# Kernel tuning notes

Hardware: AMD Instinct MI355X
Metric: run time of the kernel (lower is better)

The kernel has to match this reference:

```python
import jax, jax.numpy as jnp
import numpy as np

B, N, F = 32, 1024, 7
HID, HID_GLO, MLP_H, OUT = 256, 8, 64, 8
THRESHOLD = 0.3


def setup_inputs() -> dict:
    key = jax.random.key(0)
    ks = jax.random.split(key, 16)
    def lin(k, fan_out, fan_in):
        # xavier-uniform-like init
        lim = (6.0 / (fan_in + fan_out)) ** 0.5
        return jax.random.uniform(k, (fan_out, fan_in), jnp.float32, -lim, lim)
    return {
        "x": jax.random.normal(ks[0], (B, N, F), jnp.float32),
        "W1": lin(ks[1], HID, 2),   "b1": jnp.zeros((HID,), jnp.float32),
        "W2": lin(ks[2], HID, HID), "b2": jnp.zeros((HID,), jnp.float32),
        "Wfc": lin(ks[3], HID, HID), "bfc": jnp.zeros((HID,), jnp.float32),
        "Wg": lin(ks[4], HID_GLO, 2), "bg": jnp.zeros((HID_GLO,), jnp.float32),
        "Wm0": lin(ks[5], MLP_H, N * F), "bm0": jnp.zeros((MLP_H,), jnp.float32),
        "Wm1": lin(ks[6], MLP_H, MLP_H), "bm1": jnp.zeros((MLP_H,), jnp.float32),
        "Wp": lin(ks[7], OUT, MLP_H + HID + HID_GLO), "bp": jnp.zeros((OUT,), jnp.float32),
    }


def reference(x, W1, b1, W2, b2, Wfc, bfc, Wg, bg, Wm0, bm0, Wm1, bm1, Wp, bp):
    # --- GCN branch (torch code detaches node features & adjacency) ---
    pts = jax.lax.stop_gradient(x[:, :, 1:3])                     # [B,N,2]
    diff = pts[:, :, None, :] - pts[:, None, :, :]                # [B,N,N,2]
    dist = jnp.sqrt(jnp.sum(diff * diff, axis=-1))                # [B,N,N]
    adj = (dist < THRESHOLD).astype(x.dtype)                      # [B,N,N]
    dinv = 1.0 / jnp.sqrt(jnp.sum(adj, axis=-1))                  # [B,N] (>=1, self-loop)
    nadj = dinv[:, :, None] * adj * dinv[:, None, :]              # D^-1/2 A D^-1/2
    h = jax.nn.relu(jnp.einsum('bij,bjd->bid', nadj, pts) @ W1.T + b1)   # [B,N,256]
    g = jnp.einsum('bij,bjh->bih', nadj, h) @ W2.T + b2                  # [B,N,256]
    gcn_en = jnp.mean(g, axis=1) @ Wfc.T + bfc                    # [B,256]

    # --- global branch (torch code uses .item() -> constants) ---
    v = jax.lax.stop_gradient(x[:, :, 1:5])                       # [B,N,4]
    avg_speed = jnp.mean(jnp.linalg.norm(v[:, :, 2:4], axis=-1), axis=1)  # [B]
    density = 1.0 / jnp.max(dist, axis=(1, 2))                    # [B] (v3 == pts)
    glo_in = jnp.stack([avg_speed, density], axis=-1)             # [B,2]
    glo_en = jax.nn.relu(glo_in @ Wg.T + bg)                      # [B,8]

    # --- MLP branch on flattened x ---
    xf = x.reshape(x.shape[0], -1)                                # [B, N*F]
    xf = jax.nn.relu(xf @ Wm0.T + bm0)
    xf = jax.nn.relu(xf @ Wm1.T + bm1)                            # [B,64]

    out = jnp.concatenate([xf, gcn_en, glo_en], axis=1) @ Wp.T + bp  # [B,8]
    return out
```

## Files before the change

### kernel.cpp

```cpp
#include <hip/hip_runtime.h>

#define NN 1024
#define FF 7
#define HID 256
#define MLPH 64
#define OUTN 8
#define CATN (MLPH + HID + 8)

__device__ __forceinline__ float wave_sum(float v) {
#pragma unroll
    for (int m = 32; m >= 1; m >>= 1) v += __shfl_xor(v, m, 64);
    return v;
}
__device__ __forceinline__ float wave_max(float v) {
#pragma unroll
    for (int m = 32; m >= 1; m >>= 1) v = fmaxf(v, __shfl_xor(v, m, 64));
    return v;
}

__global__ __launch_bounds__(512, 4) void g1(const float* __restrict__ x,
                                             const float* __restrict__ Wm0,
                                             const float* __restrict__ W2,
                                             const float* __restrict__ b2,
                                             const float* __restrict__ Wfc,
                                             const float* __restrict__ bfc,
                                             const float* __restrict__ Wp,
                                             float* __restrict__ spd,
                                             float* __restrict__ mlp_p,
                                             float* __restrict__ E,
                                             float* __restrict__ cE,
                                             float* __restrict__ deg,
                                             float* __restrict__ bmaxp,
                                             float* __restrict__ out) {
    __shared__ __align__(16) float l0[NN];
    __shared__ __align__(16) float l1[NN];
    __shared__ __align__(16) float s2[8 * 128];
    __shared__ float wred[8];
    __shared__ float eg0[HID];
    __shared__ float eg1[HID];
    int blk = blockIdx.x, tid = threadIdx.x, lane = tid & 63, w = tid >> 6;
    int b = blk >> 3, jg = blk & 7;
    const float* xb = x + b * (NN * FF);
    {
        int j0 = tid, j1 = tid + 512;
        l0[j0] = xb[j0 * FF + 1]; l1[j0] = xb[j0 * FF + 2];
        l0[j1] = xb[j1 * FF + 1]; l1[j1] = xb[j1 * FF + 2];
    }
    __syncthreads();
    int jA = jg * 128 + lane, jB = jA + 64;
    float pj0a = l0[jA], pj1a = l1[jA];
    float pj0b = l0[jB], pj1b = l1[jB];
    const float4* v0p = (const float4*)&l0[w * 128];
    const float4* v1p = (const float4*)&l1[w * 128];
    unsigned dA = 0u, dB = 0u;
    float mx = 0.f;
#pragma unroll 4
    for (int g = 0; g < 32; ++g) {
        float4 v0 = v0p[g], v1 = v1p[g];
        float dx, dy, d2a, d2b;
        dx = pj0a - v0.x; dy = pj1a - v1.x; d2a = fmaf(dy, dy, dx * dx);
        dx = pj0b - v0.x; dy = pj1b - v1.x; d2b = fmaf(dy, dy, dx * dx);
        dA += (d2a <= 0.09f); dB += (d2b <= 0.09f);
        mx = fmaxf(mx, fmaxf(d2a, d2b));
        dx = pj0a - v0.y; dy = pj1a - v1.y; d2a = fmaf(dy, dy, dx * dx);
        dx = pj0b - v0.y; dy = pj1b - v1.y; d2b = fmaf(dy, dy, dx * dx);
        dA += (d2a <= 0.09f); dB += (d2b <= 0.09f);
        mx = fmaxf(mx, fmaxf(d2a, d2b));
        dx = pj0a - v0.z; dy = pj1a - v1.z; d2a = fmaf(dy, dy, dx * dx);
        dx = pj0b - v0.z; dy = pj1b - v1.z; d2b = fmaf(dy, dy, dx * dx);
        dA += (d2a <= 0.09f); dB += (d2b <= 0.09f);
        mx = fmaxf(mx, fmaxf(d2a, d2b));
        dx = pj0a - v0.w; dy = pj1a - v1.w; d2a = fmaf(dy, dy, dx * dx);
        dx = pj0b - v0.w; dy = pj1b - v1.w; d2b = fmaf(dy, dy, dx * dx);
        dA += (d2a <= 0.09f); dB += (d2b <= 0.09f);
        mx = fmaxf(mx, fmaxf(d2a, d2b));
    }
    s2[w * 128 + lane] = (float)dA;
    s2[w * 128 + 64 + lane] = (float)dB;
    mx = wave_max(mx);
    if (lane == 0) wred[w] = mx;
    __syncthreads();
    if (tid < 128) {
        float s = 0.f;
#pragma unroll
        for (int kk = 0; kk < 8; ++kk) s += s2[kk * 128 + tid];
        deg[b * NN + jg * 128 + tid] = s;
    }
    if (tid == 0) {
        float m = wred[0];
#pragma unroll
        for (int i = 1; i < 8; ++i) m = fmaxf(m, wred[i]);
        bmaxp[b * 8 + jg] = m;
    }
    {
        int h = jg * 8 + w;
        const float4* wr = (const float4*)(Wm0 + h * (NN * FF));
        const float4* xr = (const float4*)xb;
        float4 a4 = {0.f, 0.f, 0.f, 0.f};
#pragma unroll 7
        for (int it = 0; it < 28; ++it) {
            float4 wv = wr[it * 64 + lane];
            float4 xv = xr[it * 64 + lane];
            a4.x = fmaf(wv.x, xv.x, a4.x);
            a4.y = fmaf(wv.y, xv.y, a4.y);
            a4.z = fmaf(wv.z, xv.z, a4.z);
            a4.w = fmaf(wv.w, xv.w, a4.w);
        }
        float s = (a4.x + a4.y) + (a4.z + a4.w);
        s = wave_sum(s);
        if (lane == 0) mlp_p[b * MLPH + h] = s;
    }
    __syncthreads();
    if (jg == 0) {
        int j0 = tid, j1 = tid + 512;
        float vx = xb[j0 * FF + 3], vy = xb[j0 * FF + 4];
        float sp = sqrtf(fmaf(vx, vx, vy * vy));
        vx = xb[j1 * FF + 3]; vy = xb[j1 * FF + 4];
        sp += sqrtf(fmaf(vx, vx, vy * vy));
        sp = wave_sum(sp);
        if (lane == 0) wred[w] = sp;
        if (tid < OUTN) out[b * OUTN + tid] = 0.f;
    }
    __syncthreads();
    if (jg == 0 && tid == 0) {
        float s = 0.f;
#pragma unroll
        for (int i = 0; i < 8; ++i) s += wred[i];
        spd[b] = s;
    }
    if (b < 8 && jg == 7) {
        int o = b;
        if (tid < HID) eg0[tid] = Wp[o * CATN + MLPH + tid];
        __syncthreads();
        if (tid < HID) {
            float a = 0.f;
#pragma unroll 8
            for (int m = 0; m < HID; ++m) a = fmaf(eg0[m], Wfc[m * HID + tid], a);
            eg1[tid] = a;
        }
        __syncthreads();
        if (tid < HID) {
            float e = 0.f;
#pragma unroll 8
            for (int k = 0; k < HID; ++k) e = fmaf(eg1[k], W2[k * HID + tid], e);
            E[o * HID + tid] = e;
            float c = fmaf(eg1[tid], b2[tid], eg0[tid] * bfc[tid]);
            c = wave_sum(c);
            if (lane == 0) wred[w] = c;
        }
        __syncthreads();
        if (tid == 0) cE[o] = wred[0] + wred[1] + wred[2] + wred[3];
    }
}

__global__ __launch_bounds__(512, 4) void g2(const float* __restrict__ x,
                                             const float* __restrict__ deg,
                                             const float* __restrict__ W1,
                                             const float* __restrict__ b1,
                                             const float* __restrict__ Wg,
                                             const float* __restrict__ bg,
                                             const float* __restrict__ Wm1,
                                             const float* __restrict__ bm1,
                                             const float* __restrict__ Wp,
                                             const float* __restrict__ bp,
                                             const float* __restrict__ bm0,
                                             const float* __restrict__ mlp_p,
                                             const float* __restrict__ bmaxp,
                                             const float* __restrict__ spd,
                                             const float* __restrict__ E,
                                             const float* __restrict__ cE,
                                             float* __restrict__ out) {
    __shared__ __align__(16) float l0[NN];
    __shared__ __align__(16) float l1[NN];
    __shared__ __align__(16) float di[NN];
    __shared__ __align__(16) float r0[8 * 128];
    __shared__ __align__(16) float r1[8 * 128];
    __shared__ __align__(16) float r2[8 * 128];
    __shared__ __align__(16) float q0s[128];
    __shared__ __align__(16) float q1s[128];
    __shared__ __align__(16) float qws[128];
    __shared__ __align__(16) float hp[512];
    __shared__ float sx1[MLPH], sxf2[MLPH], sglo[8];
    int blk = blockIdx.x, tid = threadIdx.x, lane = tid & 63, w = tid >> 6;
    int b = blk >> 3, jg = blk & 7;
    const float* xb = x + b * (NN * FF);
    {
        int j0 = tid, j1 = tid + 512;
        l0[j0] = xb[j0 * FF + 1]; l1[j0] = xb[j0 * FF + 2];
        l0[j1] = xb[j1 * FF + 1]; l1[j1] = xb[j1 * FF + 2];
        di[j0] = 1.0f / sqrtf(deg[b * NN + j0]);
        di[j1] = 1.0f / sqrtf(deg[b * NN + j1]);
    }
    __syncthreads();
    int jA = jg * 128 + lane, jB = jA + 64;
    float pj0a = l0[jA], pj1a = l1[jA];
    float pj0b = l0[jB], pj1b = l1[jB];
    const float4* v0p = (const float4*)&l0[w * 128];
    const float4* v1p = (const float4*)&l1[w * 128];
    const float4* vdp = (const float4*)&di[w * 128];
    float a0a = 0.f, a1a = 0.f, asa = 0.f;
    float a0b = 0.f, a1b = 0.f, asb = 0.f;
#pragma unroll 4
    for (int g = 0; g < 32; ++g) {
        float4 v0 = v0p[g], v1 = v1p[g], vd = vdp[g];
        float dx, dy, d2, t;
        dx = pj0a - v0.x; dy = pj1a - v1.x; d2 = fmaf(dy, dy, dx * dx);
        t = (d2 <= 0.09f) ? vd.x : 0.0f;
        a0a = fmaf(t, v0.x, a0a); a1a = fmaf(t, v1.x, a1a); asa += t;
        dx = pj0b - v0.x; dy = pj1b - v1.x; d2 = fmaf(dy, dy, dx * dx);
        t = (d2 <= 0.09f) ? vd.x : 0.0f;
        a0b = fmaf(t, v0.x, a0b); a1b = fmaf(t, v1.x, a1b); asb += t;
        dx = pj0a - v0.y; dy = pj1a - v1.y; d2 = fmaf(dy, dy, dx * dx);
        t = (d2 <= 0.09f) ? vd.y : 0.0f;
        a0a = fmaf(t, v0.y, a0a); a1a = fmaf(t, v1.y, a1a); asa += t;
        dx = pj0b - v0.y; dy = pj1b - v1.y; d2 = fmaf(dy, dy, dx * dx);
        t = (d2 <= 0.09f) ? vd.y : 0.0f;
        a0b = fmaf(t, v0.y, a0b); a1b = fmaf(t, v1.y, a1b); asb += t;
        dx = pj0a - v0.z; dy = pj1a - v1.z; d2 = fmaf(dy, dy, dx * dx);
        t = (d2 <= 0.09f) ? vd.z : 0.0f;
        a0a = fmaf(t, v0.z, a0a); a1a = fmaf(t, v1.z, a1a); asa += t;
        dx = pj0b - v0.z; dy = pj1b - v1.z; d2 = fmaf(dy, dy, dx * dx);
        t = (d2 <= 0.09f) ? vd.z : 0.0f;
        a0b = fmaf(t, v0.z, a0b); a1b = fmaf(t, v1.z, a1b); asb += t;
        dx = pj0a - v0.w; dy = pj1a - v1.w; d2 = fmaf(dy, dy, dx * dx);
        t = (d2 <= 0.09f) ? vd.w : 0.0f;
        a0a = fmaf(t, v0.w, a0a); a1a = fmaf(t, v1.w, a1a); asa += t;
        dx = pj0b - v0.w; dy = pj1b - v1.w; d2 = fmaf(dy, dy, dx * dx);
        t = (d2 <= 0.09f) ? vd.w : 0.0f;
        a0b = fmaf(t, v0.w, a0b); a1b = fmaf(t, v1.w, a1b); asb += t;
    }
    r0[w * 128 + lane] = a0a; r0[w * 128 + 64 + lane] = a0b;
    r1[w * 128 + lane] = a1a; r1[w * 128 + 64 + lane] = a1b;
    r2[w * 128 + lane] = asa; r2[w * 128 + 64 + lane] = asb;
    __syncthreads();
    if (tid < 128) {
        float s0 = 0.f, s1 = 0.f, ss = 0.f;
#pragma unroll
        for (int kk = 0; kk < 8; ++kk) {
            s0 += r0[kk * 128 + tid];
            s1 += r1[kk * 128 + tid];
            ss += r2[kk * 128 + tid];
        }
        float dj = di[jg * 128 + tid];
        q0s[tid] = dj * s0;
        q1s[tid] = dj * s1;
        qws[tid] = dj * ss * (1.0f / NN);
    } else if (jg == 0 && tid < 192) {
        int t2 = tid - 128;
        sx1[t2] = fmaxf(mlp_p[b * MLPH + t2] + bm0[t2], 0.f);
    }
    __syncthreads();
    {
        int h = tid & 255, jq = tid >> 8;
        float w10 = W1[2 * h], w11 = W1[2 * h + 1], bb = b1[h];
        const float4* q0v = (const float4*)&q0s[jq * 64];
        const float4* q1v = (const float4*)&q1s[jq * 64];
        const float4* qwv = (const float4*)&qws[jq * 64];
        float acc = 0.f;
#pragma unroll
        for (int g = 0; g < 16; ++g) {
            float4 qa = q0v[g], qb = q1v[g], qw4 = qwv[g];
            acc = fmaf(qw4.x, fmaxf(fmaf(qb.x, w11, fmaf(qa.x, w10, bb)), 0.f), acc);
            acc = fmaf(qw4.y, fmaxf(fmaf(qb.y, w11, fmaf(qa.y, w10, bb)), 0.f), acc);
            acc = fmaf(qw4.z, fmaxf(fmaf(qb.z, w11, fmaf(qa.z, w10, bb)), 0.f), acc);
            acc = fmaf(qw4.w, fmaxf(fmaf(qb.w, w11, fmaf(qa.w, w10, bb)), 0.f), acc);
        }
        hp[jq * 256 + h] = acc;
    }
    __syncthreads();
    if (tid < HID) {
        r0[tid] = hp[tid] + hp[256 + tid];
    } else if (jg == 0 && tid < HID + MLPH) {
        int t2 = tid - HID;
        float a = bm1[t2];
        const float* wv = Wm1 + t2 * MLPH;
#pragma unroll
        for (int k = 0; k < MLPH; ++k) a = fmaf(wv[k], sx1[k], a);
        sxf2[t2] = fmaxf(a, 0.f);
    } else if (jg == 0 && tid < HID + MLPH + 8) {
        int t2 = tid - HID - MLPH;
        float mxv = 0.f;
#pragma unroll
        for (int g = 0; g < 8; ++g) mxv = fmaxf(mxv, bmaxp[b * 8 + g]);
        float avg  = spd[b] * (1.0f / NN);
        float dens = 1.0f / sqrtf(mxv);
        sglo[t2] = fmaxf(fmaf(Wg[t2 * 2], avg, fmaf(Wg[t2 * 2 + 1], dens, bg[t2])), 0.f);
    }
    __syncthreads();
    {
        int o = w, ln = lane;
        const float* Eo = E + o * HID;
        float a = Eo[ln] * r0[ln];
        a = fmaf(Eo[ln + 64],  r0[ln + 64],  a);
        a = fmaf(Eo[ln + 128], r0[ln + 128], a);
        a = fmaf(Eo[ln + 192], r0[ln + 192], a);
        if (jg == 0) a = fmaf(Wp[o * CATN + ln], sxf2[ln], a);
        a = wave_sum(a);
        if (ln == 0) {
            if (jg == 0) {
                const float* wg = Wp + o * CATN + MLPH + HID;
#pragma unroll
                for (int g = 0; g < 8; ++g) a = fmaf(wg[g], sglo[g], a);
                a += cE[o] + bp[o];
            }
            atomicAdd(&out[b * OUTN + o], a);
        }
    }
}

extern "C" void kernel_launch(void* const* d_in, const int* in_sizes, int n_in,
                              void* d_out, int out_size, void* d_ws, size_t ws_size,
                              hipStream_t stream) {
    const float* x   = (const float*)d_in[0];
    const float* W1  = (const float*)d_in[1];
    const float* b1  = (const float*)d_in[2];
    const float* W2  = (const float*)d_in[3];
    const float* b2  = (const float*)d_in[4];
    const float* Wfc = (const float*)d_in[5];
    const float* bfc = (const float*)d_in[6];
    const float* Wg  = (const float*)d_in[7];
    const float* bg  = (const float*)d_in[8];
    const float* Wm0 = (const float*)d_in[9];
    const float* bm0 = (const float*)d_in[10];
    const float* Wm1 = (const float*)d_in[11];
    const float* bm1 = (const float*)d_in[12];
    const float* Wp  = (const float*)d_in[13];
    const float* bp  = (const float*)d_in[14];
    float* out = (float*)d_out;
    float* ws  = (float*)d_ws;

    float* deg   = ws;
    float* mlp_p = ws + 32768;
    float* bmaxp = ws + 34816;
    float* spd   = ws + 35072;
    float* E     = ws + 35104;
    float* cE    = ws + 37152;

    g1<<<256, 512, 0, stream>>>(x, Wm0, W2, b2, Wfc, bfc, Wp,
                                spd, mlp_p, E, cE, deg, bmaxp, out);
    g2<<<256, 512, 0, stream>>>(x, deg, W1, b1, Wg, bg, Wm1, bm1,
                                Wp, bp, bm0, mlp_p, bmaxp, spd, E, cE, out);
}
```

Measured before the change: 124.8 us.

## Fuse two kernels into one cooperative kernel with grid sync

Merges the degree/precompute kernel and the aggregation kernel into a single cooperative launch, with a grid-wide barrier between them. The point positions stay in shared memory across the barrier and a second kernel launch is avoided. The E precompute now splits the 256-long dot products across all 512 threads in two halves and moves to blocks b 8..15. The costs are grid-sync overhead, a larger shared-memory footprint, and launch bounds lowered to 2 blocks per CU, with all 256 blocks required to be co-resident.

After: 157.7 us. 1.26x slower.

```diff
diff --git a/kernel.cpp b/kernel.cpp
--- a/kernel.cpp
+++ b/kernel.cpp
@@ -1,4 +1,7 @@
 #include <hip/hip_runtime.h>
+#include <hip/hip_cooperative_groups.h>
+
+namespace cg = cooperative_groups;
 
 #define NN 1024
 #define FF 7
@@ -18,29 +21,47 @@
     return v;
 }
 
-__global__ __launch_bounds__(512, 4) void g1(const float* __restrict__ x,
-                                             const float* __restrict__ Wm0,
-                                             const float* __restrict__ W2,
-                                             const float* __restrict__ b2,
-                                             const float* __restrict__ Wfc,
-                                             const float* __restrict__ bfc,
-                                             const float* __restrict__ Wp,
-                                             float* __restrict__ spd,
-                                             float* __restrict__ mlp_p,
-                                             float* __restrict__ E,
-                                             float* __restrict__ cE,
-                                             float* __restrict__ deg,
-                                             float* __restrict__ bmaxp,
-                                             float* __restrict__ out) {
+__global__ __launch_bounds__(512, 2) void gall(const float* __restrict__ x,
+                                               const float* __restrict__ Wm0,
+                                               const float* __restrict__ W2,
+                                               const float* __restrict__ b2,
+                                               const float* __restrict__ Wfc,
+                                               const float* __restrict__ bfc,
+                                               const float* __restrict__ W1,
+                                               const float* __restrict__ b1,
+                                               const float* __restrict__ Wg,
+                                               const float* __restrict__ bg,
+                                               const float* __restrict__ Wm1,
+                                               const float* __restrict__ bm1,
+                                               const float* __restrict__ Wp,
+                                               const float* __restrict__ bp,
+                                               const float* __restrict__ bm0,
+                                               float* __restrict__ spd,
+                                               float* __restrict__ mlp_p,
+                                               float* __restrict__ E,
+                                               float* __restrict__ cE,
+                                               float* __restrict__ deg,
+                                               float* __restrict__ bmaxp,
+                                               float* __restrict__ out) {
     __shared__ __align__(16) float l0[NN];
     __shared__ __align__(16) float l1[NN];
-    __shared__ __align__(16) float s2[8 * 128];
+    __shared__ __align__(16) float di[NN];
+    __shared__ __align__(16) float s2[NN];
+    __shared__ __align__(16) float r0[NN];
+    __shared__ __align__(16) float r1[NN];
+    __shared__ __align__(16) float r2[NN];
+    __shared__ __align__(16) float q0s[128];
+    __shared__ __align__(16) float q1s[128];
+    __shared__ __align__(16) float qws[128];
+    __shared__ __align__(16) float hp[512];
+    __shared__ float sx1[MLPH], sxf2[MLPH], sglo[8];
     __shared__ float wred[8];
-    __shared__ float eg0[HID];
-    __shared__ float eg1[HID];
+    __shared__ float eg0[HID], eg1[HID];
+
     int blk = blockIdx.x, tid = threadIdx.x, lane = tid & 63, w = tid >> 6;
     int b = blk >> 3, jg = blk & 7;
     const float* xb = x + b * (NN * FF);
+
     {
         int j0 = tid, j1 = tid + 512;
         l0[j0] = xb[j0 * FF + 1]; l1[j0] = xb[j0 * FF + 2];
@@ -50,35 +71,37 @@
     int jA = jg * 128 + lane, jB = jA + 64;
     float pj0a = l0[jA], pj1a = l1[jA];
     float pj0b = l0[jB], pj1b = l1[jB];
-    const float4* v0p = (const float4*)&l0[w * 128];
-    const float4* v1p = (const float4*)&l1[w * 128];
-    unsigned dA = 0u, dB = 0u;
-    float mx = 0.f;
+    {
+        const float4* v0p = (const float4*)&l0[w * 128];
+        const float4* v1p = (const float4*)&l1[w * 128];
+        unsigned dA = 0u, dB = 0u;
+        float mx = 0.f;
 #pragma unroll 4
-    for (int g = 0; g < 32; ++g) {
-        float4 v0 = v0p[g], v1 = v1p[g];
-        float dx, dy, d2a, d2b;
-        dx = pj0a - v0.x; dy = pj1a - v1.x; d2a = fmaf(dy, dy, dx * dx);
-        dx = pj0b - v0.x; dy = pj1b - v1.x; d2b = fmaf(dy, dy, dx * dx);
-        dA += (d2a <= 0.09f); dB += (d2b <= 0.09f);
-        mx = fmaxf(mx, fmaxf(d2a, d2b));
-        dx = pj0a - v0.y; dy = pj1a - v1.y; d2a = fmaf(dy, dy, dx * dx);
-        dx = pj0b - v0.y; dy = pj1b - v1.y; d2b = fmaf(dy, dy, dx * dx);
-        dA += (d2a <= 0.09f); dB += (d2b <= 0.09f);
-        mx = fmaxf(mx, fmaxf(d2a, d2b));
-        dx = pj0a - v0.z; dy = pj1a - v1.z; d2a = fmaf(dy, dy, dx * dx);
-        dx = pj0b - v0.z; dy = pj1b - v1.z; d2b = fmaf(dy, dy, dx * dx);
-        dA += (d2a <= 0.09f); dB += (d2b <= 0.09f);
-        mx = fmaxf(mx, fmaxf(d2a, d2b));
-        dx = pj0a - v0.w; dy = pj1a - v1.w; d2a = fmaf(dy, dy, dx * dx);
-        dx = pj0b - v0.w; dy = pj1b - v1.w; d2b = fmaf(dy, dy, dx * dx);
-        dA += (d2a <= 0.09f); dB += (d2b <= 0.09f);
-        mx = fmaxf(mx, fmaxf(d2a, d2b));
-    }
-    s2[w * 128 + lane] = (float)dA;
-    s2[w * 128 + 64 + lane] = (float)dB;
-    mx = wave_max(mx);
-    if (lane == 0) wred[w] = mx;
+        for (int g = 0; g < 32; ++g) {
+            float4 v0 = v0p[g], v1 = v1p[g];
+            float dx, dy, d2a, d2b;
+            dx = pj0a - v0.x; dy = pj1a - v1.x; d2a = fmaf(dy, dy, dx * dx);
+            dx = pj0b - v0.x; dy = pj1b - v1.x; d2b = fmaf(dy, dy, dx * dx);
+            dA += (d2a <= 0.09f); dB += (d2b <= 0.09f);
+            mx = fmaxf(mx, fmaxf(d2a, d2b));
+            dx = pj0a - v0.y; dy = pj1a - v1.y; d2a = fmaf(dy, dy, dx * dx);
+            dx = pj0b - v0.y; dy = pj1b - v1.y; d2b = fmaf(dy, dy, dx * dx);
+            dA += (d2a <= 0.09f); dB += (d2b <= 0.09f);
+            mx = fmaxf(mx, fmaxf(d2a, d2b));
+            dx = pj0a - v0.z; dy = pj1a - v1.z; d2a = fmaf(dy, dy, dx * dx);
+            dx = pj0b - v0.z; dy = pj1b - v1.z; d2b = fmaf(dy, dy, dx * dx);
+            dA += (d2a <= 0.09f); dB += (d2b <= 0.09f);
+            mx = fmaxf(mx, fmaxf(d2a, d2b));
+            dx = pj0a - v0.w; dy = pj1a - v1.w; d2a = fmaf(dy, dy, dx * dx);
+            dx = pj0b - v0.w; dy = pj1b - v1.w; d2b = fmaf(dy, dy, dx * dx);
+            dA += (d2a <= 0.09f); dB += (d2b <= 0.09f);
+            mx = fmaxf(mx, fmaxf(d2a, d2b));
+        }
+        s2[w * 128 + lane] = (float)dA;
+        s2[w * 128 + 64 + lane] = (float)dB;
+        mx = wave_max(mx);
+        if (lane == 0) wred[w] = mx;
+    }
     __syncthreads();
     if (tid < 128) {
         float s = 0.f;
@@ -128,22 +151,31 @@
         for (int i = 0; i < 8; ++i) s += wred[i];
         spd[b] = s;
     }
-    if (b < 8 && jg == 7) {
-        int o = b;
+    if (b >= 8 && b < 16 && jg == 7) {
+        int o = b - 8;
+        int half = tid >> 8, col = tid & 255;
         if (tid < HID) eg0[tid] = Wp[o * CATN + MLPH + tid];
         __syncthreads();
+        {
+            float a = 0.f;
+            const float* wcol = Wfc + (half * 128) * HID + col;
+#pragma unroll 8
+            for (int m = 0; m < 128; ++m) a = fmaf(eg0[half * 128 + m], wcol[m * HID], a);
+            hp[tid] = a;
+        }
+        __syncthreads();
+        if (tid < HID) eg1[tid] = hp[tid] + hp[tid + 256];
+        __syncthreads();
+        {
+            float e = 0.f;
+            const float* wcol = W2 + (half * 128) * HID + col;
+#pragma unroll 8
+            for (int k = 0; k < 128; ++k) e = fmaf(eg1[half * 128 + k], wcol[k * HID], e);
+            hp[tid] = e;
+        }
+        __syncthreads();
         if (tid < HID) {
-            float a = 0.f;
-#pragma unroll 8
-            for (int m = 0; m < HID; ++m) a = fmaf(eg0[m], Wfc[m * HID + tid], a);
-            eg1[tid] = a;
-        }
-        __syncthreads();
-        if (tid < HID) {
-            float e = 0.f;
-#pragma unroll 8
-            for (int k = 0; k < HID; ++k) e = fmaf(eg1[k], W2[k * HID + tid], e);
-            E[o * HID + tid] = e;
+            E[o * HID + tid] = hp[tid] + hp[tid + 256];
             float c = fmaf(eg1[tid], b2[tid], eg0[tid] * bfc[tid]);
             c = wave_sum(c);
             if (lane == 0) wred[w] = c;
@@ -151,87 +183,51 @@
         __syncthreads();
         if (tid == 0) cE[o] = wred[0] + wred[1] + wred[2] + wred[3];
     }
-}
-
-__global__ __launch_bounds__(512, 4) void g2(const float* __restrict__ x,
-                                             const float* __restrict__ deg,
-                                             const float* __restrict__ W1,
-                                             const float* __restrict__ b1,
-                                             const float* __restrict__ Wg,
-                                             const float* __restrict__ bg,
-                                             const float* __restrict__ Wm1,
-                                             const float* __restrict__ bm1,
-                                             const float* __restrict__ Wp,
-                                             const float* __restrict__ bp,
-                                             const float* __restrict__ bm0,
-                                             const float* __restrict__ mlp_p,
-                                             const float* __restrict__ bmaxp,
-                                             const float* __restrict__ spd,
-                                             const float* __restrict__ E,
-                                             const float* __restrict__ cE,
-                                             float* __restrict__ out) {
-    __shared__ __align__(16) float l0[NN];
-    __shared__ __align__(16) float l1[NN];
-    __shared__ __align__(16) float di[NN];
-    __shared__ __align__(16) float r0[8 * 128];
-    __shared__ __align__(16) float r1[8 * 128];
-    __shared__ __align__(16) float r2[8 * 128];
-    __shared__ __align__(16) float q0s[128];
-    __shared__ __align__(16) float q1s[128];
-    __shared__ __align__(16) float qws[128];
-    __shared__ __align__(16) float hp[512];
-    __shared__ float sx1[MLPH], sxf2[MLPH], sglo[8];
-    int blk = blockIdx.x, tid = threadIdx.x, lane = tid & 63, w = tid >> 6;
-    int b = blk >> 3, jg = blk & 7;
-    const float* xb = x + b * (NN * FF);
-    {
-        int j0 = tid, j1 = tid + 512;
-        l0[j0] = xb[j0 * FF + 1]; l1[j0] = xb[j0 * FF + 2];
-        l0[j1] = xb[j1 * FF + 1]; l1[j1] = xb[j1 * FF + 2];
-        di[j0] = 1.0f / sqrtf(deg[b * NN + j0]);
-        di[j1] = 1.0f / sqrtf(deg[b * NN + j1]);
-    }
-    __syncthreads();
-    int jA = jg * 128 + lane, jB = jA + 64;
-    float pj0a = l0[jA], pj1a = l1[jA];
-    float pj0b = l0[jB], pj1b = l1[jB];
-    const float4* v0p = (const float4*)&l0[w * 128];
-    const float4* v1p = (const float4*)&l1[w * 128];
-    const float4* vdp = (const float4*)&di[w * 128];
-    float a0a = 0.f, a1a = 0.f, asa = 0.f;
-    float a0b = 0.f, a1b = 0.f, asb = 0.f;
+
+    cg::this_grid().sync();
+
+    di[tid]       = 1.0f / sqrtf(deg[b * NN + tid]);
+    di[tid + 512] = 1.0f / sqrtf(deg[b * NN + tid + 512]);
+    __syncthreads();
+    {
+        const float4* v0p = (const float4*)&l0[w * 128];
+        const float4* v1p = (const float4*)&l1[w * 128];
+        const float4* vdp = (const float4*)&di[w * 128];
+        float a0a = 0.f, a1a = 0.f, asa = 0.f;
+        float a0b = 0.f, a1b = 0.f, asb = 0.f;
 #pragma unroll 4
-    for (int g = 0; g < 32; ++g) {
-        float4 v0 = v0p[g], v1 = v1p[g], vd = vdp[g];
-        float dx, dy, d2, t;
-        dx = pj0a - v0.x; dy = pj1a - v1.x; d2 = fmaf(dy, dy, dx * dx);
-        t = (d2 <= 0.09f) ? vd.x : 0.0f;
-        a0a = fmaf(t, v0.x, a0a); a1a = fmaf(t, v1.x, a1a); asa += t;
-        dx = pj0b - v0.x; dy = pj1b - v1.x; d2 = fmaf(dy, dy, dx * dx);
-        t = (d2 <= 0.09f) ? vd.x : 0.0f;
-        a0b = fmaf(t, v0.x, a0b); a1b = fmaf(t, v1.x, a1b); asb += t;
-        dx = pj0a - v0.y; dy = pj1a - v1.y; d2 = fmaf(dy, dy, dx * dx);
-        t = (d2 <= 0.09f) ? vd.y : 0.0f;
-        a0a = fmaf(t, v0.y, a0a); a1a = fmaf(t, v1.y, a1a); asa += t;
-        dx = pj0b - v0.y; dy = pj1b - v1.y; d2 = fmaf(dy, dy, dx * dx);
-        t = (d2 <= 0.09f) ? vd.y : 0.0f;
-        a0b = fmaf(t, v0.y, a0b); a1b = fmaf(t, v1.y, a1b); asb += t;
-        dx = pj0a - v0.z; dy = pj1a - v1.z; d2 = fmaf(dy, dy, dx * dx);
-        t = (d2 <= 0.09f) ? vd.z : 0.0f;
-        a0a = fmaf(t, v0.z, a0a); a1a = fmaf(t, v1.z, a1a); asa += t;
-        dx = pj0b - v0.z; dy = pj1b - v1.z; d2 = fmaf(dy, dy, dx * dx);
-        t = (d2 <= 0.09f) ? vd.z : 0.0f;
-        a0b = fmaf(t, v0.z, a0b); a1b = fmaf(t, v1.z, a1b); asb += t;
-        dx = pj0a - v0.w; dy = pj1a - v1.w; d2 = fmaf(dy, dy, dx * dx);
-        t = (d2 <= 0.09f) ? vd.w : 0.0f;
-        a0a = fmaf(t, v0.w, a0a); a1a = fmaf(t, v1.w, a1a); asa += t;
-        dx = pj0b - v0.w; dy = pj1b - v1.w; d2 = fmaf(dy, dy, dx * dx);
-        t = (d2 <= 0.09f) ? vd.w : 0.0f;
-        a0b = fmaf(t, v0.w, a0b); a1b = fmaf(t, v1.w, a1b); asb += t;
-    }
-    r0[w * 128 + lane] = a0a; r0[w * 128 + 64 + lane] = a0b;
-    r1[w * 128 + lane] = a1a; r1[w * 128 + 64 + lane] = a1b;
-    r2[w * 128 + lane] = asa; r2[w * 128 + 64 + lane] = asb;
+        for (int g = 0; g < 32; ++g) {
+            float4 v0 = v0p[g], v1 = v1p[g], vd = vdp[g];
+            float dx, dy, d2, t;
+            dx = pj0a - v0.x; dy = pj1a - v1.x; d2 = fmaf(dy, dy, dx * dx);
+            t = (d2 <= 0.09f) ? vd.x : 0.0f;
+            a0a = fmaf(t, v0.x, a0a); a1a = fmaf(t, v1.x, a1a); asa += t;
+            dx = pj0b - v0.x; dy = pj1b - v1.x; d2 = fmaf(dy, dy, dx * dx);
+            t = (d2 <= 0.09f) ? vd.x : 0.0f;
+            a0b = fmaf(t, v0.x, a0b); a1b = fmaf(t, v1.x, a1b); asb += t;
+            dx = pj0a - v0.y; dy = pj1a - v1.y; d2 = fmaf(dy, dy, dx * dx);
+            t = (d2 <= 0.09f) ? vd.y : 0.0f;
+            a0a = fmaf(t, v0.y, a0a); a1a = fmaf(t, v1.y, a1a); asa += t;
+            dx = pj0b - v0.y; dy = pj1b - v1.y; d2 = fmaf(dy, dy, dx * dx);
+            t = (d2 <= 0.09f) ? vd.y : 0.0f;
+            a0b = fmaf(t, v0.y, a0b); a1b = fmaf(t, v1.y, a1b); asb += t;
+            dx = pj0a - v0.z; dy = pj1a - v1.z; d2 = fmaf(dy, dy, dx * dx);
+            t = (d2 <= 0.09f) ? vd.z : 0.0f;
+            a0a = fmaf(t, v0.z, a0a); a1a = fmaf(t, v1.z, a1a); asa += t;
+            dx = pj0b - v0.z; dy = pj1b - v1.z; d2 = fmaf(dy, dy, dx * dx);
+            t = (d2 <= 0.09f) ? vd.z : 0.0f;
+            a0b = fmaf(t, v0.z, a0b); a1b = fmaf(t, v1.z, a1b); asb += t;
+            dx = pj0a - v0.w; dy = pj1a - v1.w; d2 = fmaf(dy, dy, dx * dx);
+            t = (d2 <= 0.09f) ? vd.w : 0.0f;
+            a0a = fmaf(t, v0.w, a0a); a1a = fmaf(t, v1.w, a1a); asa += t;
+            dx = pj0b - v0.w; dy = pj1b - v1.w; d2 = fmaf(dy, dy, dx * dx);
+            t = (d2 <= 0.09f) ? vd.w : 0.0f;
+            a0b = fmaf(t, v0.w, a0b); a1b = fmaf(t, v1.w, a1b); asb += t;
+        }
+        r0[w * 128 + lane] = a0a; r0[w * 128 + 64 + lane] = a0b;
+        r1[w * 128 + lane] = a1a; r1[w * 128 + 64 + lane] = a1b;
+        r2[w * 128 + lane] = asa; r2[w * 128 + 64 + lane] = asb;
+    }
     __syncthreads();
     if (tid < 128) {
         float s0 = 0.f, s1 = 0.f, ss = 0.f;
@@ -336,8 +332,12 @@
     float* E     = ws + 35104;
     float* cE    = ws + 37152;
 
-    g1<<<256, 512, 0, stream>>>(x, Wm0, W2, b2, Wfc, bfc, Wp,
-                                spd, mlp_p, E, cE, deg, bmaxp, out);
-    g2<<<256, 512, 0, stream>>>(x, deg, W1, b1, Wg, bg, Wm1, bm1,
-                                Wp, bp, bm0, mlp_p, bmaxp, spd, E, cE, out);
+    void* kargs[] = {(void*)&x,   (void*)&Wm0, (void*)&W2,  (void*)&b2,
+                     (void*)&Wfc, (void*)&bfc, (void*)&W1,  (void*)&b1,
+                     (void*)&Wg,  (void*)&bg,  (void*)&Wm1, (void*)&bm1,
+                     (void*)&Wp,  (void*)&bp,  (void*)&bm0,
+                     (void*)&spd, (void*)&mlp_p, (void*)&E, (void*)&cE,
+                     (void*)&deg, (void*)&bmaxp, (void*)&out};
+    hipLaunchCooperativeKernel(reinterpret_cast<void*>(gall), dim3(256), dim3(512),
+                               kargs, 0, stream);
 }
```

## Prefetch Wm0 into registers, stage x in LDS, split E-precompute across all threads

Applied to the files above, without the earlier changes.

At kernel start each wave loads its whole Wm0 row slice into 28 float4 registers, so those global loads overlap the LDS staging and the pairwise-distance loop. The batch's x slab is copied to shared memory with coalesced float4 loads, and the positions, the MLP dot product and the speed sum all read from LDS instead of strided global accesses. The Wfc/W2 chain that computes E now uses all 512 threads, each half reducing over 128 rows, and runs on blocks b=8..15 instead of 0..7. In exchange register and LDS use grow, so the occupancy hint drops from 4 to 2 blocks per CU.

Measured after the change: 113.3 us. -9.2%, faster.

```diff
diff --git a/kernel.cpp b/kernel.cpp
--- a/kernel.cpp
+++ b/kernel.cpp
@@ -18,7 +18,7 @@
     return v;
 }
 
-__global__ __launch_bounds__(512, 4) void g1(const float* __restrict__ x,
+__global__ __launch_bounds__(512, 2) void g1(const float* __restrict__ x,
                                              const float* __restrict__ Wm0,
                                              const float* __restrict__ W2,
                                              const float* __restrict__ b2,
@@ -32,53 +32,70 @@
                                              float* __restrict__ deg,
                                              float* __restrict__ bmaxp,
                                              float* __restrict__ out) {
+    __shared__ __align__(16) float lxs[NN * FF];
     __shared__ __align__(16) float l0[NN];
     __shared__ __align__(16) float l1[NN];
-    __shared__ __align__(16) float s2[8 * 128];
+    __shared__ __align__(16) float s2[NN];
     __shared__ float wred[8];
     __shared__ float eg0[HID];
     __shared__ float eg1[HID];
     int blk = blockIdx.x, tid = threadIdx.x, lane = tid & 63, w = tid >> 6;
     int b = blk >> 3, jg = blk & 7;
-    const float* xb = x + b * (NN * FF);
-    {
-        int j0 = tid, j1 = tid + 512;
-        l0[j0] = xb[j0 * FF + 1]; l1[j0] = xb[j0 * FF + 2];
-        l0[j1] = xb[j1 * FF + 1]; l1[j1] = xb[j1 * FF + 2];
-    }
+
+    const float4* wr = (const float4*)(Wm0 + (jg * 8 + w) * (NN * FF));
+    float4 wreg[28];
+#pragma unroll
+    for (int t = 0; t < 28; ++t) wreg[t] = wr[t * 64 + lane];
+    const float4* xr4 = (const float4*)(x + b * (NN * FF));
+    float4 xreg0 = xr4[tid];
+    float4 xreg1 = xr4[512 + tid];
+    float4 xreg2 = xr4[1024 + tid];
+    float4 xreg3;
+    if (tid < 256) xreg3 = xr4[1536 + tid];
+    float4* lx4 = (float4*)lxs;
+    lx4[tid] = xreg0;
+    lx4[512 + tid] = xreg1;
+    lx4[1024 + tid] = xreg2;
+    if (tid < 256) lx4[1536 + tid] = xreg3;
+    __syncthreads();
+    l0[tid] = lxs[tid * 7 + 1];       l1[tid] = lxs[tid * 7 + 2];
+    l0[tid + 512] = lxs[(tid + 512) * 7 + 1];
+    l1[tid + 512] = lxs[(tid + 512) * 7 + 2];
     __syncthreads();
     int jA = jg * 128 + lane, jB = jA + 64;
     float pj0a = l0[jA], pj1a = l1[jA];
     float pj0b = l0[jB], pj1b = l1[jB];
-    const float4* v0p = (const float4*)&l0[w * 128];
-    const float4* v1p = (const float4*)&l1[w * 128];
-    unsigned dA = 0u, dB = 0u;
-    float mx = 0.f;
+    {
+        const float4* v0p = (const float4*)&l0[w * 128];
+        const float4* v1p = (const float4*)&l1[w * 128];
+        unsigned dA = 0u, dB = 0u;
+        float mx = 0.f;
 #pragma unroll 4
-    for (int g = 0; g < 32; ++g) {
-        float4 v0 = v0p[g], v1 = v1p[g];
-        float dx, dy, d2a, d2b;
-        dx = pj0a - v0.x; dy = pj1a - v1.x; d2a = fmaf(dy, dy, dx * dx);
-        dx = pj0b - v0.x; dy = pj1b - v1.x; d2b = fmaf(dy, dy, dx * dx);
-        dA += (d2a <= 0.09f); dB += (d2b <= 0.09f);
-        mx = fmaxf(mx, fmaxf(d2a, d2b));
-        dx = pj0a - v0.y; dy = pj1a - v1.y; d2a = fmaf(dy, dy, dx * dx);
-        dx = pj0b - v0.y; dy = pj1b - v1.y; d2b = fmaf(dy, dy, dx * dx);
-        dA += (d2a <= 0.09f); dB += (d2b <= 0.09f);
-        mx = fmaxf(mx, fmaxf(d2a, d2b));
-        dx = pj0a - v0.z; dy = pj1a - v1.z; d2a = fmaf(dy, dy, dx * dx);
-        dx = pj0b - v0.z; dy = pj1b - v1.z; d2b = fmaf(dy, dy, dx * dx);
-        dA += (d2a <= 0.09f); dB += (d2b <= 0.09f);
-        mx = fmaxf(mx, fmaxf(d2a, d2b));
-        dx = pj0a - v0.w; dy = pj1a - v1.w; d2a = fmaf(dy, dy, dx * dx);
-        dx = pj0b - v0.w; dy = pj1b - v1.w; d2b = fmaf(dy, dy, dx * dx);
-        dA += (d2a <= 0.09f); dB += (d2b <= 0.09f);
-        mx = fmaxf(mx, fmaxf(d2a, d2b));
-    }
-    s2[w * 128 + lane] = (float)dA;
-    s2[w * 128 + 64 + lane] = (float)dB;
-    mx = wave_max(mx);
-    if (lane == 0) wred[w] = mx;
+        for (int g = 0; g < 32; ++g) {
+            float4 v0 = v0p[g], v1 = v1p[g];
+            float dx, dy, d2a, d2b;
+            dx = pj0a - v0.x; dy = pj1a - v1.x; d2a = fmaf(dy, dy, dx * dx);
+            dx = pj0b - v0.x; dy = pj1b - v1.x; d2b = fmaf(dy, dy, dx * dx);
+            dA += (d2a <= 0.09f); dB += (d2b <= 0.09f);
+            mx = fmaxf(mx, fmaxf(d2a, d2b));
+            dx = pj0a - v0.y; dy = pj1a - v1.y; d2a = fmaf(dy, dy, dx * dx);
+            dx = pj0b - v0.y; dy = pj1b - v1.y; d2b = fmaf(dy, dy, dx * dx);
+            dA += (d2a <= 0.09f); dB += (d2b <= 0.09f);
+            mx = fmaxf(mx, fmaxf(d2a, d2b));
+            dx = pj0a - v0.z; dy = pj1a - v1.z; d2a = fmaf(dy, dy, dx * dx);
+            dx = pj0b - v0.z; dy = pj1b - v1.z; d2b = fmaf(dy, dy, dx * dx);
+            dA += (d2a <= 0.09f); dB += (d2b <= 0.09f);
+            mx = fmaxf(mx, fmaxf(d2a, d2b));
+            dx = pj0a - v0.w; dy = pj1a - v1.w; d2a = fmaf(dy, dy, dx * dx);
+            dx = pj0b - v0.w; dy = pj1b - v1.w; d2b = fmaf(dy, dy, dx * dx);
+            dA += (d2a <= 0.09f); dB += (d2b <= 0.09f);
+            mx = fmaxf(mx, fmaxf(d2a, d2b));
+        }
+        s2[w * 128 + lane] = (float)dA;
+        s2[w * 128 + 64 + lane] = (float)dB;
+        mx = wave_max(mx);
+        if (lane == 0) wred[w] = mx;
+    }
     __syncthreads();
     if (tid < 128) {
         float s = 0.f;
@@ -93,29 +110,24 @@
         bmaxp[b * 8 + jg] = m;
     }
     {
-        int h = jg * 8 + w;
-        const float4* wr = (const float4*)(Wm0 + h * (NN * FF));
-        const float4* xr = (const float4*)xb;
         float4 a4 = {0.f, 0.f, 0.f, 0.f};
-#pragma unroll 7
-        for (int it = 0; it < 28; ++it) {
-            float4 wv = wr[it * 64 + lane];
-            float4 xv = xr[it * 64 + lane];
-            a4.x = fmaf(wv.x, xv.x, a4.x);
-            a4.y = fmaf(wv.y, xv.y, a4.y);
-            a4.z = fmaf(wv.z, xv.z, a4.z);
-            a4.w = fmaf(wv.w, xv.w, a4.w);
+#pragma unroll
+        for (int t = 0; t < 28; ++t) {
+            float4 xv = lx4[t * 64 + lane];
+            a4.x = fmaf(wreg[t].x, xv.x, a4.x);
+            a4.y = fmaf(wreg[t].y, xv.y, a4.y);
+            a4.z = fmaf(wreg[t].z, xv.z, a4.z);
+            a4.w = fmaf(wreg[t].w, xv.w, a4.w);
         }
         float s = (a4.x + a4.y) + (a4.z + a4.w);
         s = wave_sum(s);
-        if (lane == 0) mlp_p[b * MLPH + h] = s;
+        if (lane == 0) mlp_p[b * MLPH + jg * 8 + w] = s;
     }
     __syncthreads();
     if (jg == 0) {
-        int j0 = tid, j1 = tid + 512;
-        float vx = xb[j0 * FF + 3], vy = xb[j0 * FF + 4];
+        float vx = lxs[tid * 7 + 3], vy = lxs[tid * 7 + 4];
         float sp = sqrtf(fmaf(vx, vx, vy * vy));
-        vx = xb[j1 * FF + 3]; vy = xb[j1 * FF + 4];
+        vx = lxs[(tid + 512) * 7 + 3]; vy = lxs[(tid + 512) * 7 + 4];
         sp += sqrtf(fmaf(vx, vx, vy * vy));
         sp = wave_sum(sp);
         if (lane == 0) wred[w] = sp;
@@ -128,22 +140,32 @@
         for (int i = 0; i < 8; ++i) s += wred[i];
         spd[b] = s;
     }
-    if (b < 8 && jg == 7) {
-        int o = b;
+    if (b >= 8 && b < 16 && jg == 7) {
+        int o = b - 8;
+        int half = tid >> 8, col = tid & 255;
+        float* hp = s2;
         if (tid < HID) eg0[tid] = Wp[o * CATN + MLPH + tid];
         __syncthreads();
+        {
+            float a = 0.f;
+            const float* wcol = Wfc + (half * 128) * HID + col;
+#pragma unroll 8
+            for (int m = 0; m < 128; ++m) a = fmaf(eg0[half * 128 + m], wcol[m * HID], a);
+            hp[tid] = a;
+        }
+        __syncthreads();
+        if (tid < HID) eg1[tid] = hp[tid] + hp[tid + 256];
+        __syncthreads();
+        {
+            float e = 0.f;
+            const float* wcol = W2 + (half * 128) * HID + col;
+#pragma unroll 8
+            for (int k = 0; k < 128; ++k) e = fmaf(eg1[half * 128 + k], wcol[k * HID], e);
+            hp[tid] = e;
+        }
+        __syncthreads();
         if (tid < HID) {
-            float a = 0.f;
-#pragma unroll 8
-            for (int m = 0; m < HID; ++m) a = fmaf(eg0[m], Wfc[m * HID + tid], a);
-            eg1[tid] = a;
-        }
-        __syncthreads();
-        if (tid < HID) {
-            float e = 0.f;
-#pragma unroll 8
-            for (int k = 0; k < HID; ++k) e = fmaf(eg1[k], W2[k * HID + tid], e);
-            E[o * HID + tid] = e;
+            E[o * HID + tid] = hp[tid] + hp[tid + 256];
             float c = fmaf(eg1[tid], b2[tid], eg0[tid] * bfc[tid]);
             c = wave_sum(c);
             if (lane == 0) wred[w] = c;
```
